# Optimization experiments

Measured on AMD Instinct MI355X. Metric: run time of the kernel, lower is better.

Reference implementation:

```python
import jax, jax.numpy as jnp
import numpy as np

D = 192      # d_model
DE = 96      # d_edge
H = 8        # n_heads
DH = D // H  # d_head = 24
DF = 2 * D   # ff hidden = 384
N = 25000
E = 400000


def _layernorm(x, s, b, eps=1e-5):
    m = jnp.mean(x, axis=-1, keepdims=True)
    v = jnp.var(x, axis=-1, keepdims=True)
    return (x - m) * jax.lax.rsqrt(v + eps) * s + b


def setup_inputs() -> dict:
    key = jax.random.key(0)
    ks = jax.random.split(key, 12)
    sc = lambda d: 1.0 / np.sqrt(d)
    inp = {
        "x": jax.random.normal(ks[0], (N, D), jnp.float32),
        "edge_feat": jax.random.normal(ks[1], (E, DE), jnp.float32),
        "edge_index": jax.random.randint(ks[2], (2, E), 0, N, jnp.int64),
        # attention projections (stored [d_in, d_out], applied as x @ W)
        "Wq": jax.random.normal(ks[3], (D, D), jnp.float32) * sc(D),
        "Wk": jax.random.normal(ks[4], (D, D), jnp.float32) * sc(D),
        "Wv": jax.random.normal(ks[5], (D, D), jnp.float32) * sc(D),
        "We": jax.random.normal(ks[6], (DE, H), jnp.float32) * sc(DE),
        "Wo": jax.random.normal(ks[7], (D, D), jnp.float32) * sc(D),
        "bo": jnp.zeros((D,), jnp.float32),
        "Wg": jax.random.normal(ks[8], (2 * D, D), jnp.float32) * sc(2 * D),
        "bg": jnp.zeros((D,), jnp.float32),
        "ln1_s": jnp.ones((D,), jnp.float32),
        "ln1_b": jnp.zeros((D,), jnp.float32),
        "Wf1": jax.random.normal(ks[9], (D, DF), jnp.float32) * sc(D),
        "bf1": jnp.zeros((DF,), jnp.float32),
        "Wf2": jax.random.normal(ks[10], (DF, D), jnp.float32) * sc(DF),
        "bf2": jnp.zeros((D,), jnp.float32),
        "ln2_s": jnp.ones((D,), jnp.float32),
        "ln2_b": jnp.zeros((D,), jnp.float32),
    }
    return inp


def reference(x, edge_feat, edge_index, Wq, Wk, Wv, We, Wo, bo, Wg, bg,
              ln1_s, ln1_b, Wf1, bf1, Wf2, bf2, ln2_s, ln2_b):
    src, dst = edge_index[0], edge_index[1]
    n = x.shape[0]
    # per-edge gathered projections: [E, H, DH]
    q = (x[dst] @ Wq).reshape(-1, H, DH)
    k = (x[src] @ Wk).reshape(-1, H, DH)
    v = (x[src] @ Wv).reshape(-1, H, DH)
    score = jnp.sum(q * k, axis=-1) / np.sqrt(DH) + edge_feat @ We  # [E, H]
    # segment softmax over incoming edges of each dst node
    mx = jax.ops.segment_max(score, dst, num_segments=n)           # [N, H]
    alpha = jnp.exp(score - mx[dst])                                # [E, H]
    den = jax.ops.segment_sum(alpha, dst, num_segments=n)          # [N, H]
    num = jax.ops.segment_sum(alpha[..., None] * v, dst, num_segments=n)  # [N, H, DH]
    agg = (num / (den[:, :, None] + 1e-8)).reshape(n, D)
    o = agg @ Wo + bo
    g = jax.nn.sigmoid(jnp.concatenate([o, x], axis=-1) @ Wg + bg)
    y = _layernorm(g * o + (1.0 - g) * x, ln1_s, ln1_b)
    ff = jax.nn.silu(y @ Wf1 + bf1) @ Wf2 + bf2
    return _layernorm(y + ff, ln2_s, ln2_b)
```

## Files before the change

kernel.cpp:

```cpp
#include <hip/hip_runtime.h>
#include <cstdint>
#include <cstddef>

#define LOG2E 1.4426950408889634f

constexpr int Dm  = 192;
constexpr int DEe = 96;

typedef unsigned short u16;
typedef __attribute__((ext_vector_type(8))) short short8v;
typedef __attribute__((ext_vector_type(4))) float f32x4;

__device__ __forceinline__ u16 f2bf(float f) {
    uint32_t u = __builtin_bit_cast(uint32_t, f);
    uint32_t r = (u + 0x7FFF + ((u >> 16) & 1)) >> 16;
    return (u16)r;
}
__device__ __forceinline__ float bf2f(u16 h) {
    uint32_t u = ((uint32_t)h) << 16;
    return __builtin_bit_cast(float, u);
}

__global__ void zero_ints(int* __restrict__ p, int n) {
    int i = blockIdx.x * blockDim.x + threadIdx.x;
    if (i < n) p[i] = 0;
}

__global__ void count_deg(const int* __restrict__ ei, int E, int* __restrict__ deg) {
    int e = blockIdx.x * blockDim.x + threadIdx.x;
    if (e < E) atomicAdd(&deg[ei[E + e]], 1);
}

__global__ __launch_bounds__(1024) void scan_kernel(const int* __restrict__ deg, int N,
                                                    int* __restrict__ offs) {
    __shared__ int sp[1024];
    int t = threadIdx.x;
    int per = (N + 1023) >> 10;
    int base = t * per;
    int sum = 0;
    for (int i = 0; i < per; ++i) {
        int idx = base + i;
        if (idx < N) sum += deg[idx];
    }
    sp[t] = sum;
    __syncthreads();
    for (int off = 1; off < 1024; off <<= 1) {
        int v = (t >= off) ? sp[t - off] : 0;
        __syncthreads();
        sp[t] += v;
        __syncthreads();
    }
    int run = sp[t] - sum;
    for (int i = 0; i < per; ++i) {
        int idx = base + i;
        if (idx < N) { offs[idx] = run; run += deg[idx]; }
    }
    if (t == 1023) offs[N] = sp[1023];
}

__global__ void xconv(const float* __restrict__ x, int n4, u16* __restrict__ xb) {
    int i = blockIdx.x * blockDim.x + threadIdx.x;
    if (i >= n4) return;
    float4 v = ((const float4*)x)[i];
    ushort4 o;
    o.x = f2bf(v.x); o.y = f2bf(v.y); o.z = f2bf(v.z); o.w = f2bf(v.w);
    ((ushort4*)xb)[i] = o;
}

__global__ void prep_w(const float* __restrict__ Wq, const float* __restrict__ Wk,
                       const float* __restrict__ Wv, const float* __restrict__ Wo,
                       const float* __restrict__ Wg, const float* __restrict__ Wf1,
                       const float* __restrict__ Wf2,
                       u16* __restrict__ Wqkvt, u16* __restrict__ Wot,
                       u16* __restrict__ Wgt, u16* __restrict__ Wf1t,
                       u16* __restrict__ Wf2t) {
    int idx = blockIdx.x * blockDim.x + threadIdx.x;
    if (idx < 110592) {
        int n = idx / 192, k = idx % 192;
        const float* W = n < 192 ? Wq : (n < 384 ? Wk : Wv);
        Wqkvt[idx] = f2bf(W[(size_t)k * 192 + (n % 192)]);
    } else if (idx < 147456) {
        int i = idx - 110592;
        int n = i / 192, k = i % 192;
        Wot[i] = f2bf(Wo[(size_t)k * 192 + n]);
    } else if (idx < 221184) {
        int i = idx - 147456;
        int n = i / 384, k = i % 384;
        Wgt[i] = f2bf(Wg[(size_t)k * 192 + n]);
    } else if (idx < 294912) {
        int i = idx - 221184;
        int n = i / 192, k = i % 192;
        Wf1t[i] = f2bf(Wf1[(size_t)k * 384 + n]);
    } else if (idx < 368640) {
        int i = idx - 294912;
        int n = i / 384, k = i % 384;
        Wf2t[i] = f2bf(Wf2[(size_t)k * 192 + n]);
    }
}

__global__ __launch_bounds__(256) void edge_prep(
    const int* __restrict__ ei, int E,
    const float* __restrict__ ef, const float* __restrict__ We,
    const int* __restrict__ offs, int* __restrict__ cur,
    float* __restrict__ scb, int* __restrict__ sbuf)
{
    __shared__ float We_s[DEe * 8];
    __shared__ float ef_s[32][100];
    int tid = threadIdx.x;
    for (int i = tid; i < DEe * 8; i += 256) We_s[i] = We[i];
    int e0 = blockIdx.x * 32;
    #pragma unroll
    for (int rep = 0; rep < 3; ++rep) {
        int idx = tid + 256 * rep;
        int el = idx / 24, c4 = idx % 24;
        int e = e0 + el;
        float4 v = make_float4(0.f, 0.f, 0.f, 0.f);
        if (e < E) v = *(const float4*)&ef[(size_t)e * DEe + c4 * 4];
        *(float4*)&ef_s[el][c4 * 4] = v;
    }
    __syncthreads();
    int el = tid >> 3, h = tid & 7;
    int e = e0 + el;
    if (e >= E) return;
    float epj = 0.f;
    #pragma unroll 8
    for (int i = 0; i < DEe; ++i) epj += ef_s[el][i] * We_s[i * 8 + h];

    int lane = tid & 63;
    int pos = 0;
    if (h == 0) {
        int dst = ei[E + e];
        pos = offs[dst] + atomicAdd(&cur[dst], 1);
    }
    pos = __shfl(pos, lane & 56, 64);
    scb[(size_t)pos * 8 + h] = epj * LOG2E;
    if (h == 0) sbuf[pos] = ei[e];
}

__global__ __launch_bounds__(256) void agg_fused(
    const u16* __restrict__ qkv, const float* __restrict__ scb,
    const int* __restrict__ sbuf, const int* __restrict__ offs,
    int N, u16* __restrict__ aggb)
{
    int node = blockIdx.x * 4 + (threadIdx.x >> 6);
    if (node >= N) return;
    int lane = threadIdx.x & 63;
    int h = lane >> 3;
    int di = (3 * lane) >> 1;
    int odd = lane & 1;

    const uint32_t* qrow = (const uint32_t*)(qkv + (size_t)node * 576);
    uint32_t qd0 = qrow[di], qd1 = qrow[di + 1];
    float q0, q1, q2;
    if (!odd) { q0 = bf2f(qd0 & 0xffff); q1 = bf2f(qd0 >> 16); q2 = bf2f(qd1 & 0xffff); }
    else      { q0 = bf2f(qd0 >> 16);    q1 = bf2f(qd1 & 0xffff); q2 = bf2f(qd1 >> 16); }

    float den = 0.f, a0 = 0.f, a1 = 0.f, a2 = 0.f;
    int beg = offs[node], end = offs[node + 1];

    uint32_t kd0_n = 0, kd1_n = 0, vd0_n = 0, vd1_n = 0; float ep_n = 0.f;
    if (beg < end) {
        int src = sbuf[beg];
        const uint32_t* kr = (const uint32_t*)(qkv + (size_t)src * 576 + 192);
        kd0_n = kr[di]; kd1_n = kr[di + 1];
        const uint32_t* vr = (const uint32_t*)(qkv + (size_t)src * 576 + 384);
        vd0_n = vr[di]; vd1_n = vr[di + 1];
        ep_n = scb[(size_t)beg * 8 + h];
    }

    for (int idx = beg; idx < end; ++idx) {
        uint32_t kd0 = kd0_n, kd1 = kd1_n, vd0 = vd0_n, vd1 = vd1_n;
        float ep = ep_n;
        if (idx + 1 < end) {
            int src = sbuf[idx + 1];
            const uint32_t* kr = (const uint32_t*)(qkv + (size_t)src * 576 + 192);
            kd0_n = kr[di]; kd1_n = kr[di + 1];
            const uint32_t* vr = (const uint32_t*)(qkv + (size_t)src * 576 + 384);
            vd0_n = vr[di]; vd1_n = vr[di + 1];
            ep_n = scb[(size_t)(idx + 1) * 8 + h];
        }
        float k0, k1, k2, v0, v1, v2;
        if (!odd) {
            k0 = bf2f(kd0 & 0xffff); k1 = bf2f(kd0 >> 16); k2 = bf2f(kd1 & 0xffff);
            v0 = bf2f(vd0 & 0xffff); v1 = bf2f(vd0 >> 16); v2 = bf2f(vd1 & 0xffff);
        } else {
            k0 = bf2f(kd0 >> 16); k1 = bf2f(kd1 & 0xffff); k2 = bf2f(kd1 >> 16);
            v0 = bf2f(vd0 >> 16); v1 = bf2f(vd1 & 0xffff); v2 = bf2f(vd1 >> 16);
        }
        float pd = q0 * k0 + q1 * k1 + q2 * k2;
        pd += __shfl_xor(pd, 1, 64);
        pd += __shfl_xor(pd, 2, 64);
        pd += __shfl_xor(pd, 4, 64);
        float p = exp2f(pd * 0.2944885836f + ep);
        den += p;
        a0 += p * v0; a1 += p * v1; a2 += p * v2;
    }
    float rden = 1.f / (den + 1e-8f);
    u16* og = aggb + (size_t)node * Dm;
    int b0 = 3 * lane;
    og[b0]     = f2bf(a0 * rden);
    og[b0 + 1] = f2bf(a1 * rden);
    og[b0 + 2] = f2bf(a2 * rden);
}

__global__ __launch_bounds__(512) void qkv_gemm(
    const u16* __restrict__ xb, int M,
    const u16* __restrict__ Wt, u16* __restrict__ qkvb)
{
    int tid = threadIdx.x;
    int m0 = blockIdx.x * 128, n0 = blockIdx.y * 192;
    int w = tid >> 6, lane = tid & 63;
    int wr = w >> 2, wc = w & 3;
    int c16 = lane & 15, hi2 = lane >> 4, kof = hi2 * 8;
    int rbase = m0 + wr * 64;

    int rcm[4];
    #pragma unroll
    for (int mr = 0; mr < 4; ++mr) {
        int r = rbase + mr * 16 + c16;
        rcm[mr] = r < M ? r : M - 1;
    }

    f32x4 acc[4][3];
    #pragma unroll
    for (int mr = 0; mr < 4; ++mr)
        #pragma unroll
        for (int nr = 0; nr < 3; ++nr) acc[mr][nr] = (f32x4)(0.f);

    #pragma unroll 1
    for (int ks = 0; ks < 6; ++ks) {
        short8v af[4], bfr[3];
        #pragma unroll
        for (int mr = 0; mr < 4; ++mr)
            af[mr] = *(const short8v*)(xb + (size_t)rcm[mr] * 192 + ks * 32 + kof);
        #pragma unroll
        for (int nr = 0; nr < 3; ++nr)
            bfr[nr] = *(const short8v*)(Wt + (size_t)(n0 + wc * 48 + nr * 16 + c16) * 192 + ks * 32 + kof);
        #pragma unroll
        for (int mr = 0; mr < 4; ++mr)
            #pragma unroll
            for (int nr = 0; nr < 3; ++nr)
                acc[mr][nr] = __builtin_amdgcn_mfma_f32_16x16x32_bf16(
                    af[mr], bfr[nr], acc[mr][nr], 0, 0, 0);
    }

    #pragma unroll
    for (int mr = 0; mr < 4; ++mr)
        #pragma unroll
        for (int reg = 0; reg < 4; ++reg) {
            int r = rbase + mr * 16 + hi2 * 4 + reg;
            if (r >= M) continue;
            #pragma unroll
            for (int nr = 0; nr < 3; ++nr)
                qkvb[(size_t)r * 576 + n0 + wc * 48 + nr * 16 + c16] =
                    f2bf(acc[mr][nr][reg]);
        }
}

__global__ __launch_bounds__(512) void chain_fused(
    const u16* __restrict__ aggb, const u16* __restrict__ xb, int M,
    const u16* __restrict__ Wot, const float* __restrict__ bo,
    const u16* __restrict__ Wgt, const float* __restrict__ bg,
    const float* __restrict__ l1s, const float* __restrict__ l1b,
    const u16* __restrict__ Wf1t, const float* __restrict__ bf1,
    const u16* __restrict__ Wf2t, const float* __restrict__ bf2,
    const float* __restrict__ l2s, const float* __restrict__ l2b,
    float* __restrict__ out)
{
    __shared__ __align__(16) short Ybuf[128 * 200];
    __shared__ __align__(16) short Fbuf[128 * 392];
    __shared__ float red[2][4][128];

    int tid = threadIdx.x;
    int m0 = blockIdx.x * 128;
    int w = tid >> 6, lane = tid & 63;
    int wr = w >> 2, wc = w & 3;
    int c16 = lane & 15, hi2 = lane >> 4, kof = hi2 * 8;
    int rbase = m0 + wr * 64;
    int lbase = wr * 64;

    int rcm[4];
    #pragma unroll
    for (int mr = 0; mr < 4; ++mr) {
        int r = rbase + mr * 16 + c16;
        rcm[mr] = r < M ? r : M - 1;
    }

    f32x4 oacc[4][3];
    #pragma unroll
    for (int mr = 0; mr < 4; ++mr)
        #pragma unroll
        for (int nr = 0; nr < 3; ++nr) oacc[mr][nr] = (f32x4)(0.f);
    #pragma unroll 1
    for (int ks = 0; ks < 6; ++ks) {
        short8v af[4], bfr[3];
        #pragma unroll
        for (int mr = 0; mr < 4; ++mr)
            af[mr] = *(const short8v*)(aggb + (size_t)rcm[mr] * 192 + ks * 32 + kof);
        #pragma unroll
        for (int nr = 0; nr < 3; ++nr)
            bfr[nr] = *(const short8v*)(Wot + (size_t)(wc * 48 + nr * 16 + c16) * 192 + ks * 32 + kof);
        #pragma unroll
        for (int mr = 0; mr < 4; ++mr)
            #pragma unroll
            for (int nr = 0; nr < 3; ++nr)
                oacc[mr][nr] = __builtin_amdgcn_mfma_f32_16x16x32_bf16(
                    af[mr], bfr[nr], oacc[mr][nr], 0, 0, 0);
    }
    #pragma unroll
    for (int nr = 0; nr < 3; ++nr) {
        int col = wc * 48 + nr * 16 + c16;
        float b = bo[col];
        #pragma unroll
        for (int mr = 0; mr < 4; ++mr)
            #pragma unroll
            for (int reg = 0; reg < 4; ++reg) {
                oacc[mr][nr][reg] += b;
                int row = lbase + mr * 16 + hi2 * 4 + reg;
                Ybuf[row * 200 + col] = (short)f2bf(oacc[mr][nr][reg]);
            }
    }
    __syncthreads();

    f32x4 zacc[4][3];
    #pragma unroll
    for (int mr = 0; mr < 4; ++mr)
        #pragma unroll
        for (int nr = 0; nr < 3; ++nr) zacc[mr][nr] = (f32x4)(0.f);
    #pragma unroll 1
    for (int ks = 0; ks < 6; ++ks) {
        short8v af[4], bfr[3];
        #pragma unroll
        for (int mr = 0; mr < 4; ++mr)
            af[mr] = *(const short8v*)&Ybuf[(lbase + mr * 16 + c16) * 200 + ks * 32 + kof];
        #pragma unroll
        for (int nr = 0; nr < 3; ++nr)
            bfr[nr] = *(const short8v*)(Wgt + (size_t)(wc * 48 + nr * 16 + c16) * 384 + ks * 32 + kof);
        #pragma unroll
        for (int mr = 0; mr < 4; ++mr)
            #pragma unroll
            for (int nr = 0; nr < 3; ++nr)
                zacc[mr][nr] = __builtin_amdgcn_mfma_f32_16x16x32_bf16(
                    af[mr], bfr[nr], zacc[mr][nr], 0, 0, 0);
    }
    #pragma unroll 1
    for (int ks = 0; ks < 6; ++ks) {
        short8v af[4], bfr[3];
        #pragma unroll
        for (int mr = 0; mr < 4; ++mr)
            af[mr] = *(const short8v*)(xb + (size_t)rcm[mr] * 192 + ks * 32 + kof);
        #pragma unroll
        for (int nr = 0; nr < 3; ++nr)
            bfr[nr] = *(const short8v*)(Wgt + (size_t)(wc * 48 + nr * 16 + c16) * 384 + 192 + ks * 32 + kof);
        #pragma unroll
        for (int mr = 0; mr < 4; ++mr)
            #pragma unroll
            for (int nr = 0; nr < 3; ++nr)
                zacc[mr][nr] = __builtin_amdgcn_mfma_f32_16x16x32_bf16(
                    af[mr], bfr[nr], zacc[mr][nr], 0, 0, 0);
    }
    float s1p[4][4], s2p[4][4];
    #pragma unroll
    for (int mr = 0; mr < 4; ++mr)
        #pragma unroll
        for (int reg = 0; reg < 4; ++reg) {
            int gr = rbase + mr * 16 + hi2 * 4 + reg;
            int rcR = gr < M ? gr : M - 1;
            float s1 = 0.f, s2 = 0.f;
            #pragma unroll
            for (int nr = 0; nr < 3; ++nr) {
                int col = wc * 48 + nr * 16 + c16;
                float z = zacc[mr][nr][reg] + bg[col];
                float g = 1.f / (1.f + expf(-z));
                float xv = bf2f(xb[(size_t)rcR * 192 + col]);
                float val = g * oacc[mr][nr][reg] + (1.f - g) * xv;
                zacc[mr][nr][reg] = val;
                s1 += val; s2 += val * val;
            }
            #pragma unroll
            for (int mS = 1; mS < 16; mS <<= 1) {
                s1 += __shfl_xor(s1, mS, 64);
                s2 += __shfl_xor(s2, mS, 64);
            }
            s1p[mr][reg] = s1; s2p[mr][reg] = s2;
        }
    if (c16 == 0) {
        #pragma unroll
        for (int mr = 0; mr < 4; ++mr)
            #pragma unroll
            for (int reg = 0; reg < 4; ++reg) {
                int rowIdx = lbase + mr * 16 + hi2 * 4 + reg;
                red[0][wc][rowIdx] = s1p[mr][reg];
                red[1][wc][rowIdx] = s2p[mr][reg];
            }
    }
    __syncthreads();
    #pragma unroll
    for (int mr = 0; mr < 4; ++mr)
        #pragma unroll
        for (int reg = 0; reg < 4; ++reg) {
            int rowIdx = lbase + mr * 16 + hi2 * 4 + reg;
            float S1 = red[0][0][rowIdx] + red[0][1][rowIdx] + red[0][2][rowIdx] + red[0][3][rowIdx];
            float S2 = red[1][0][rowIdx] + red[1][1][rowIdx] + red[1][2][rowIdx] + red[1][3][rowIdx];
            float mean = S1 * (1.f / 192.f);
            float var  = S2 * (1.f / 192.f) - mean * mean;
            float inv  = rsqrtf(var + 1e-5f);
            #pragma unroll
            for (int nr = 0; nr < 3; ++nr) {
                int col = wc * 48 + nr * 16 + c16;
                float yv = (zacc[mr][nr][reg] - mean) * inv * l1s[col] + l1b[col];
                Ybuf[rowIdx * 200 + col] = (short)f2bf(yv);
            }
        }
    __syncthreads();

    f32x4 tacc[4][6];
    #pragma unroll
    for (int mr = 0; mr < 4; ++mr)
        #pragma unroll
        for (int nr = 0; nr < 6; ++nr) tacc[mr][nr] = (f32x4)(0.f);
    #pragma unroll 1
    for (int ks = 0; ks < 6; ++ks) {
        short8v af[4], bfr[6];
        #pragma unroll
        for (int mr = 0; mr < 4; ++mr)
            af[mr] = *(const short8v*)&Ybuf[(lbase + mr * 16 + c16) * 200 + ks * 32 + kof];
        #pragma unroll
        for (int nr = 0; nr < 6; ++nr)
            bfr[nr] = *(const short8v*)(Wf1t + (size_t)(wc * 96 + nr * 16 + c16) * 192 + ks * 32 + kof);
        #pragma unroll
        for (int mr = 0; mr < 4; ++mr)
            #pragma unroll
            for (int nr = 0; nr < 6; ++nr)
                tacc[mr][nr] = __builtin_amdgcn_mfma_f32_16x16x32_bf16(
                    af[mr], bfr[nr], tacc[mr][nr], 0, 0, 0);
    }
    #pragma unroll
    for (int nr = 0; nr < 6; ++nr) {
        int col = wc * 96 + nr * 16 + c16;
        float b = bf1[col];
        #pragma unroll
        for (int mr = 0; mr < 4; ++mr)
            #pragma unroll
            for (int reg = 0; reg < 4; ++reg) {
                float z = tacc[mr][nr][reg] + b;
                float t = z / (1.f + expf(-z));
                int row = lbase + mr * 16 + hi2 * 4 + reg;
                Fbuf[row * 392 + col] = (short)f2bf(t);
            }
    }
    __syncthreads();

    f32x4 facc[4][3];
    #pragma unroll
    for (int mr = 0; mr < 4; ++mr)
        #pragma unroll
        for (int nr = 0; nr < 3; ++nr) facc[mr][nr] = (f32x4)(0.f);
    #pragma unroll 1
    for (int ks = 0; ks < 12; ++ks) {
        short8v af[4], bfr[3];
        #pragma unroll
        for (int mr = 0; mr < 4; ++mr)
            af[mr] = *(const short8v*)&Fbuf[(lbase + mr * 16 + c16) * 392 + ks * 32 + kof];
        #pragma unroll
        for (int nr = 0; nr < 3; ++nr)
            bfr[nr] = *(const short8v*)(Wf2t + (size_t)(wc * 48 + nr * 16 + c16) * 384 + ks * 32 + kof);
        #pragma unroll
        for (int mr = 0; mr < 4; ++mr)
            #pragma unroll
            for (int nr = 0; nr < 3; ++nr)
                facc[mr][nr] = __builtin_amdgcn_mfma_f32_16x16x32_bf16(
                    af[mr], bfr[nr], facc[mr][nr], 0, 0, 0);
    }
    float s1q[4][4], s2q[4][4];
    #pragma unroll
    for (int mr = 0; mr < 4; ++mr)
        #pragma unroll
        for (int reg = 0; reg < 4; ++reg) {
            int rowIdx = lbase + mr * 16 + hi2 * 4 + reg;
            float s1 = 0.f, s2 = 0.f;
            #pragma unroll
            for (int nr = 0; nr < 3; ++nr) {
                int col = wc * 48 + nr * 16 + c16;
                float val = facc[mr][nr][reg] + bf2[col] + bf2f((u16)Ybuf[rowIdx * 200 + col]);
                facc[mr][nr][reg] = val;
                s1 += val; s2 += val * val;
            }
            #pragma unroll
            for (int mS = 1; mS < 16; mS <<= 1) {
                s1 += __shfl_xor(s1, mS, 64);
                s2 += __shfl_xor(s2, mS, 64);
            }
            s1q[mr][reg] = s1; s2q[mr][reg] = s2;
        }
    if (c16 == 0) {
        #pragma unroll
        for (int mr = 0; mr < 4; ++mr)
            #pragma unroll
            for (int reg = 0; reg < 4; ++reg) {
                int rowIdx = lbase + mr * 16 + hi2 * 4 + reg;
                red[0][wc][rowIdx] = s1q[mr][reg];
                red[1][wc][rowIdx] = s2q[mr][reg];
            }
    }
    __syncthreads();
    #pragma unroll
    for (int mr = 0; mr < 4; ++mr)
        #pragma unroll
        for (int reg = 0; reg < 4; ++reg) {
            int rowIdx = lbase + mr * 16 + hi2 * 4 + reg;
            int r = m0 + rowIdx;
            if (r >= M) continue;
            float S1 = red[0][0][rowIdx] + red[0][1][rowIdx] + red[0][2][rowIdx] + red[0][3][rowIdx];
            float S2 = red[1][0][rowIdx] + red[1][1][rowIdx] + red[1][2][rowIdx] + red[1][3][rowIdx];
            float mean = S1 * (1.f / 192.f);
            float var  = S2 * (1.f / 192.f) - mean * mean;
            float inv  = rsqrtf(var + 1e-5f);
            #pragma unroll
            for (int nr = 0; nr < 3; ++nr) {
                int col = wc * 48 + nr * 16 + c16;
                out[(size_t)r * 192 + col] =
                    (facc[mr][nr][reg] - mean) * inv * l2s[col] + l2b[col];
            }
        }
}

extern "C" void kernel_launch(void* const* d_in, const int* in_sizes, int n_in,
                              void* d_out, int out_size, void* d_ws, size_t ws_size,
                              hipStream_t stream) {
    const float* x   = (const float*)d_in[0];
    const float* ef  = (const float*)d_in[1];
    const int*   ei  = (const int*)d_in[2];
    const float* Wq  = (const float*)d_in[3];
    const float* Wk  = (const float*)d_in[4];
    const float* Wv  = (const float*)d_in[5];
    const float* We  = (const float*)d_in[6];
    const float* Wo  = (const float*)d_in[7];
    const float* bo  = (const float*)d_in[8];
    const float* Wg  = (const float*)d_in[9];
    const float* bg  = (const float*)d_in[10];
    const float* l1s = (const float*)d_in[11];
    const float* l1b = (const float*)d_in[12];
    const float* Wf1 = (const float*)d_in[13];
    const float* bf1 = (const float*)d_in[14];
    const float* Wf2 = (const float*)d_in[15];
    const float* bf2 = (const float*)d_in[16];
    const float* l2s = (const float*)d_in[17];
    const float* l2b = (const float*)d_in[18];

    int N = in_sizes[0] / Dm;
    int E = in_sizes[1] / DEe;
    float* out = (float*)d_out;

    char* wp = (char*)d_ws;
    auto alloc = [&](size_t bytes) -> void* {
        void* p = wp;
        wp += (bytes + 255) & ~(size_t)255;
        return p;
    };
    size_t NF = (size_t)N * Dm;
    u16*   xb     = (u16*)alloc(NF * 2);
    u16*   qkvb   = (u16*)alloc((size_t)N * 576 * 2);
    u16*   aggb   = (u16*)alloc(NF * 2);
    float* scb    = (float*)alloc((size_t)E * 8 * 4);
    int*   sbuf   = (int*)  alloc((size_t)E * 4);
    int*   degcur = (int*)  alloc((size_t)2 * N * 4);
    int*   offs   = (int*)  alloc((size_t)(N + 1) * 4);
    u16*   Wqkvt  = (u16*)alloc((size_t)576 * 192 * 2);
    u16*   Wot    = (u16*)alloc((size_t)192 * 192 * 2);
    u16*   Wgt    = (u16*)alloc((size_t)192 * 384 * 2);
    u16*   Wf1t   = (u16*)alloc((size_t)384 * 192 * 2);
    u16*   Wf2t   = (u16*)alloc((size_t)192 * 384 * 2);
    int* deg = degcur;
    int* cur = degcur + N;

    int gm128 = (N + 127) / 128;

    prep_w<<<dim3(1440), 256, 0, stream>>>(Wq, Wk, Wv, Wo, Wg, Wf1, Wf2,
        Wqkvt, Wot, Wgt, Wf1t, Wf2t);
    xconv<<<dim3((N * Dm / 4 + 255) / 256), 256, 0, stream>>>(x, N * Dm / 4, xb);
    zero_ints<<<dim3((2 * N + 255) / 256), 256, 0, stream>>>(degcur, 2 * N);
    count_deg<<<dim3((E + 255) / 256), 256, 0, stream>>>(ei, E, deg);
    scan_kernel<<<dim3(1), 1024, 0, stream>>>(deg, N, offs);

    qkv_gemm<<<dim3(gm128, 3), 512, 0, stream>>>(xb, N, Wqkvt, qkvb);

    edge_prep<<<dim3((E + 31) / 32), 256, 0, stream>>>(ei, E, ef, We,
        offs, cur, scb, sbuf);
    agg_fused<<<dim3((N + 3) / 4), 256, 0, stream>>>(qkvb, scb, sbuf, offs, N, aggb);

    chain_fused<<<dim3(gm128), 512, 0, stream>>>(aggb, xb, N,
        Wot, bo, Wgt, bg, l1s, l1b, Wf1t, bf1, Wf2t, bf2, l2s, l2b, out);
}
```

Measured before the change: 285.9 us.

## Deepen edge prefetch in aggregation and use packed bf16 conversion instruction

The aggregation kernel now handles two edges per iteration and prefetches the K/V rows and edge scores two edges ahead, plus source indices further ahead. Out-of-range slots are clamped and masked, and zero-degree nodes exit early. Separately, the software float-to-bf16 rounding is replaced with the hardware v_cvt_pk_bf16_f32 instruction in xconv, qkv_gemm and the chain_fused epilogues. The goal is to hide gather latency and cut conversion ALU work, at the cost of more registers and redundant clamped loads for odd-degree nodes.

```diff
diff --git a/kernel.cpp b/kernel.cpp
--- a/kernel.cpp
+++ b/kernel.cpp
@@ -19,6 +19,11 @@
 __device__ __forceinline__ float bf2f(u16 h) {
     uint32_t u = ((uint32_t)h) << 16;
     return __builtin_bit_cast(float, u);
+}
+__device__ __forceinline__ uint32_t cvtpk_bf16(float lo, float hi) {
+    uint32_t r;
+    asm("v_cvt_pk_bf16_f32 %0, %1, %2" : "=v"(r) : "v"(lo), "v"(hi));
+    return r;
 }
 
 __global__ void zero_ints(int* __restrict__ p, int n) {
@@ -62,8 +67,11 @@
     int i = blockIdx.x * blockDim.x + threadIdx.x;
     if (i >= n4) return;
     float4 v = ((const float4*)x)[i];
+    uint32_t p0 = cvtpk_bf16(v.x, v.y);
+    uint32_t p1 = cvtpk_bf16(v.z, v.w);
     ushort4 o;
-    o.x = f2bf(v.x); o.y = f2bf(v.y); o.z = f2bf(v.z); o.w = f2bf(v.w);
+    o.x = (u16)(p0 & 0xffff); o.y = (u16)(p0 >> 16);
+    o.z = (u16)(p1 & 0xffff); o.w = (u16)(p1 >> 16);
     ((ushort4*)xb)[i] = o;
 }
 
@@ -149,55 +157,100 @@
     int di = (3 * lane) >> 1;
     int odd = lane & 1;
 
+    int beg = offs[node], end = offs[node + 1];
+    u16* og = aggb + (size_t)node * Dm;
+    int b0 = 3 * lane;
+    if (beg >= end) {
+        og[b0] = 0; og[b0 + 1] = 0; og[b0 + 2] = 0;
+        return;
+    }
+
     const uint32_t* qrow = (const uint32_t*)(qkv + (size_t)node * 576);
     uint32_t qd0 = qrow[di], qd1 = qrow[di + 1];
     float q0, q1, q2;
     if (!odd) { q0 = bf2f(qd0 & 0xffff); q1 = bf2f(qd0 >> 16); q2 = bf2f(qd1 & 0xffff); }
     else      { q0 = bf2f(qd0 >> 16);    q1 = bf2f(qd1 & 0xffff); q2 = bf2f(qd1 >> 16); }
 
+    auto clampi = [&](int i) { return i < end ? i : end - 1; };
+
     float den = 0.f, a0 = 0.f, a1 = 0.f, a2 = 0.f;
-    int beg = offs[node], end = offs[node + 1];
-
-    uint32_t kd0_n = 0, kd1_n = 0, vd0_n = 0, vd1_n = 0; float ep_n = 0.f;
-    if (beg < end) {
-        int src = sbuf[beg];
-        const uint32_t* kr = (const uint32_t*)(qkv + (size_t)src * 576 + 192);
-        kd0_n = kr[di]; kd1_n = kr[di + 1];
-        const uint32_t* vr = (const uint32_t*)(qkv + (size_t)src * 576 + 384);
-        vd0_n = vr[di]; vd1_n = vr[di + 1];
-        ep_n = scb[(size_t)beg * 8 + h];
-    }
-
-    for (int idx = beg; idx < end; ++idx) {
-        uint32_t kd0 = kd0_n, kd1 = kd1_n, vd0 = vd0_n, vd1 = vd1_n;
-        float ep = ep_n;
-        if (idx + 1 < end) {
-            int src = sbuf[idx + 1];
-            const uint32_t* kr = (const uint32_t*)(qkv + (size_t)src * 576 + 192);
-            kd0_n = kr[di]; kd1_n = kr[di + 1];
-            const uint32_t* vr = (const uint32_t*)(qkv + (size_t)src * 576 + 384);
-            vd0_n = vr[di]; vd1_n = vr[di + 1];
-            ep_n = scb[(size_t)(idx + 1) * 8 + h];
-        }
-        float k0, k1, k2, v0, v1, v2;
-        if (!odd) {
-            k0 = bf2f(kd0 & 0xffff); k1 = bf2f(kd0 >> 16); k2 = bf2f(kd1 & 0xffff);
-            v0 = bf2f(vd0 & 0xffff); v1 = bf2f(vd0 >> 16); v2 = bf2f(vd1 & 0xffff);
-        } else {
-            k0 = bf2f(kd0 >> 16); k1 = bf2f(kd1 & 0xffff); k2 = bf2f(kd1 >> 16);
-            v0 = bf2f(vd0 >> 16); v1 = bf2f(vd1 & 0xffff); v2 = bf2f(vd1 >> 16);
-        }
-        float pd = q0 * k0 + q1 * k1 + q2 * k2;
-        pd += __shfl_xor(pd, 1, 64);
-        pd += __shfl_xor(pd, 2, 64);
-        pd += __shfl_xor(pd, 4, 64);
-        float p = exp2f(pd * 0.2944885836f + ep);
-        den += p;
-        a0 += p * v0; a1 += p * v1; a2 += p * v2;
-    }
+
+    uint32_t ck[2][2], cv[2][2]; float cep[2];
+    uint32_t nk[2][2], nv[2][2]; float nep[2];
+    int s0, s1;
+
+    {
+        int p00 = clampi(beg),     p01 = clampi(beg + 1);
+        int p10 = clampi(beg + 2), p11 = clampi(beg + 3);
+        int sA = sbuf[p00], sB = sbuf[p01], sC = sbuf[p10], sD = sbuf[p11];
+        const uint32_t* r;
+        r = (const uint32_t*)(qkv + (size_t)sA * 576 + 192);
+        ck[0][0] = r[di]; ck[0][1] = r[di + 1];
+        r = (const uint32_t*)(qkv + (size_t)sA * 576 + 384);
+        cv[0][0] = r[di]; cv[0][1] = r[di + 1];
+        r = (const uint32_t*)(qkv + (size_t)sB * 576 + 192);
+        ck[1][0] = r[di]; ck[1][1] = r[di + 1];
+        r = (const uint32_t*)(qkv + (size_t)sB * 576 + 384);
+        cv[1][0] = r[di]; cv[1][1] = r[di + 1];
+        r = (const uint32_t*)(qkv + (size_t)sC * 576 + 192);
+        nk[0][0] = r[di]; nk[0][1] = r[di + 1];
+        r = (const uint32_t*)(qkv + (size_t)sC * 576 + 384);
+        nv[0][0] = r[di]; nv[0][1] = r[di + 1];
+        r = (const uint32_t*)(qkv + (size_t)sD * 576 + 192);
+        nk[1][0] = r[di]; nk[1][1] = r[di + 1];
+        r = (const uint32_t*)(qkv + (size_t)sD * 576 + 384);
+        nv[1][0] = r[di]; nv[1][1] = r[di + 1];
+        cep[0] = scb[(size_t)p00 * 8 + h]; cep[1] = scb[(size_t)p01 * 8 + h];
+        nep[0] = scb[(size_t)p10 * 8 + h]; nep[1] = scb[(size_t)p11 * 8 + h];
+        s0 = sbuf[clampi(beg + 4)]; s1 = sbuf[clampi(beg + 5)];
+    }
+
+    for (int idx = beg; idx < end; idx += 2) {
+        #pragma unroll
+        for (int j = 0; j < 2; ++j) {
+            float k0, k1, k2, v0, v1, v2;
+            uint32_t kd0 = ck[j][0], kd1 = ck[j][1];
+            uint32_t vd0 = cv[j][0], vd1 = cv[j][1];
+            if (!odd) {
+                k0 = bf2f(kd0 & 0xffff); k1 = bf2f(kd0 >> 16); k2 = bf2f(kd1 & 0xffff);
+                v0 = bf2f(vd0 & 0xffff); v1 = bf2f(vd0 >> 16); v2 = bf2f(vd1 & 0xffff);
+            } else {
+                k0 = bf2f(kd0 >> 16); k1 = bf2f(kd1 & 0xffff); k2 = bf2f(kd1 >> 16);
+                v0 = bf2f(vd0 >> 16); v1 = bf2f(vd1 & 0xffff); v2 = bf2f(vd1 >> 16);
+            }
+            float pd = q0 * k0 + q1 * k1 + q2 * k2;
+            pd += __shfl_xor(pd, 1, 64);
+            pd += __shfl_xor(pd, 2, 64);
+            pd += __shfl_xor(pd, 4, 64);
+            float p = exp2f(pd * 0.2944885836f + cep[j]);
+            if (idx + j < end) {
+                den += p;
+                a0 += p * v0; a1 += p * v1; a2 += p * v2;
+            }
+        }
+        #pragma unroll
+        for (int j = 0; j < 2; ++j) {
+            ck[j][0] = nk[j][0]; ck[j][1] = nk[j][1];
+            cv[j][0] = nv[j][0]; cv[j][1] = nv[j][1];
+            cep[j] = nep[j];
+        }
+        {
+            const uint32_t* r;
+            r = (const uint32_t*)(qkv + (size_t)s0 * 576 + 192);
+            nk[0][0] = r[di]; nk[0][1] = r[di + 1];
+            r = (const uint32_t*)(qkv + (size_t)s0 * 576 + 384);
+            nv[0][0] = r[di]; nv[0][1] = r[di + 1];
+            r = (const uint32_t*)(qkv + (size_t)s1 * 576 + 192);
+            nk[1][0] = r[di]; nk[1][1] = r[di + 1];
+            r = (const uint32_t*)(qkv + (size_t)s1 * 576 + 384);
+            nv[1][0] = r[di]; nv[1][1] = r[di + 1];
+            nep[0] = scb[(size_t)clampi(idx + 4) * 8 + h];
+            nep[1] = scb[(size_t)clampi(idx + 5) * 8 + h];
+        }
+        s0 = sbuf[clampi(idx + 6)]; s1 = sbuf[clampi(idx + 7)];
+    }
+
     float rden = 1.f / (den + 1e-8f);
-    u16* og = aggb + (size_t)node * Dm;
-    int b0 = 3 * lane;
     og[b0]     = f2bf(a0 * rden);
     og[b0 + 1] = f2bf(a1 * rden);
     og[b0 + 2] = f2bf(a2 * rden);
@@ -247,13 +300,15 @@
     #pragma unroll
     for (int mr = 0; mr < 4; ++mr)
         #pragma unroll
-        for (int reg = 0; reg < 4; ++reg) {
-            int r = rbase + mr * 16 + hi2 * 4 + reg;
-            if (r >= M) continue;
-            #pragma unroll
-            for (int nr = 0; nr < 3; ++nr)
-                qkvb[(size_t)r * 576 + n0 + wc * 48 + nr * 16 + c16] =
-                    f2bf(acc[mr][nr][reg]);
+        for (int nr = 0; nr < 3; ++nr) {
+            uint32_t p0 = cvtpk_bf16(acc[mr][nr][0], acc[mr][nr][1]);
+            uint32_t p1 = cvtpk_bf16(acc[mr][nr][2], acc[mr][nr][3]);
+            int r0 = rbase + mr * 16 + hi2 * 4;
+            int col = n0 + wc * 48 + nr * 16 + c16;
+            if (r0     < M) qkvb[(size_t)(r0    ) * 576 + col] = (u16)(p0 & 0xffff);
+            if (r0 + 1 < M) qkvb[(size_t)(r0 + 1) * 576 + col] = (u16)(p0 >> 16);
+            if (r0 + 2 < M) qkvb[(size_t)(r0 + 2) * 576 + col] = (u16)(p1 & 0xffff);
+            if (r0 + 3 < M) qkvb[(size_t)(r0 + 3) * 576 + col] = (u16)(p1 >> 16);
         }
 }
 
@@ -312,13 +367,17 @@
         int col = wc * 48 + nr * 16 + c16;
         float b = bo[col];
         #pragma unroll
-        for (int mr = 0; mr < 4; ++mr)
-            #pragma unroll
-            for (int reg = 0; reg < 4; ++reg) {
-                oacc[mr][nr][reg] += b;
-                int row = lbase + mr * 16 + hi2 * 4 + reg;
-                Ybuf[row * 200 + col] = (short)f2bf(oacc[mr][nr][reg]);
-            }
+        for (int mr = 0; mr < 4; ++mr) {
+            #pragma unroll
+            for (int reg = 0; reg < 4; ++reg) oacc[mr][nr][reg] += b;
+            uint32_t p0 = cvtpk_bf16(oacc[mr][nr][0], oacc[mr][nr][1]);
+            uint32_t p1 = cvtpk_bf16(oacc[mr][nr][2], oacc[mr][nr][3]);
+            int row0 = lbase + mr * 16 + hi2 * 4;
+            Ybuf[(row0    ) * 200 + col] = (short)(p0 & 0xffff);
+            Ybuf[(row0 + 1) * 200 + col] = (short)(p0 >> 16);
+            Ybuf[(row0 + 2) * 200 + col] = (short)(p1 & 0xffff);
+            Ybuf[(row0 + 3) * 200 + col] = (short)(p1 >> 16);
+        }
     }
     __syncthreads();
 
@@ -440,14 +499,21 @@
         int col = wc * 96 + nr * 16 + c16;
         float b = bf1[col];
         #pragma unroll
-        for (int mr = 0; mr < 4; ++mr)
+        for (int mr = 0; mr < 4; ++mr) {
+            float t0[4];
             #pragma unroll
             for (int reg = 0; reg < 4; ++reg) {
                 float z = tacc[mr][nr][reg] + b;
-                float t = z / (1.f + expf(-z));
-                int row = lbase + mr * 16 + hi2 * 4 + reg;
-                Fbuf[row * 392 + col] = (short)f2bf(t);
-            }
+                t0[reg] = z / (1.f + expf(-z));
+            }
+            uint32_t p0 = cvtpk_bf16(t0[0], t0[1]);
+            uint32_t p1 = cvtpk_bf16(t0[2], t0[3]);
+            int row0 = lbase + mr * 16 + hi2 * 4;
+            Fbuf[(row0    ) * 392 + col] = (short)(p0 & 0xffff);
+            Fbuf[(row0 + 1) * 392 + col] = (short)(p0 >> 16);
+            Fbuf[(row0 + 2) * 392 + col] = (short)(p1 & 0xffff);
+            Fbuf[(row0 + 3) * 392 + col] = (short)(p1 >> 16);
+        }
     }
     __syncthreads();
 
```

Measured after the change: 277.4 us. 1.03x faster.
